# Performance work log

Measured on AMD Instinct MI355X. Metric: run time of the kernel, lower is better.

The kernel has to match this reference:

```python
import jax, jax.numpy as jnp
import numpy as np

SCALE = 8
NUM_CLASSES = 15
IGNORE_THRES = 0.5
# anchors for scale=8 divided by scale
GRID_ANCHOR = jnp.array([[96.0 / 8, 230.0 / 8], [79.0 / 8, 186.0 / 8], [81.0 / 8, 133.0 / 8]], dtype=jnp.float32)  # [3,2]


def _bce_sum(p, t, mask):
    # torch BCELoss(reduction='sum') with log clamped at -100, restricted to mask
    lp = jnp.maximum(jnp.log(p), -100.0)
    ln = jnp.maximum(jnp.log(1.0 - p), -100.0)
    return jnp.sum(-(t * lp + (1.0 - t) * ln) * mask)


def setup_inputs() -> dict:
    key = jax.random.key(0)
    k1, k2, k3 = jax.random.split(key, 3)
    nB, nG = 128, 52
    x = jax.random.normal(k1, (nB, 3 * (NUM_CLASSES + 5), nG, nG), dtype=jnp.float32)
    boxes = jax.random.uniform(k2, (nB, 4), minval=0.1, maxval=0.6)  # cx,cy,w,h in (0,1)
    cls = jax.random.randint(k3, (nB, 1), 0, NUM_CLASSES).astype(jnp.float32)
    labels = jnp.concatenate([boxes, cls], axis=-1)  # [nB,5]
    return {"x": x, "labels": labels}


def reference(x, labels):
    nB, nG = x.shape[0], x.shape[2]
    pred = x.reshape(nB, 3, NUM_CLASSES + 5, nG, nG).transpose(0, 1, 3, 4, 2)  # [B,3,G,G,20]
    px = jax.nn.sigmoid(pred[..., 0])
    py = jax.nn.sigmoid(pred[..., 1])
    pw = pred[..., 2]
    ph = pred[..., 3]
    conf = jax.nn.sigmoid(pred[..., 4])
    cls = jax.nn.softmax(pred[..., 5:], axis=-1)
    pred_boxs = jnp.stack([px, py, pw, ph], axis=-1)  # [B,3,G,G,4]
    out = jnp.concatenate([
        pred_boxs.reshape(nB, -1, 4) * SCALE,
        conf.reshape(nB, -1, 1),
        cls.reshape(nB, -1, NUM_CLASSES),
    ], axis=-1)

    # ---- build_targets (vectorized; one target per image as in original loop) ----
    tb = labels[:, :4] * nG  # boxes in grid units [B,4]
    gx, gy, gw, gh = tb[:, 0], tb[:, 1], tb[:, 2], tb[:, 3]
    gi = gx.astype(jnp.int32)
    gj = gy.astype(jnp.int32)
    gcls = labels[:, 4].astype(jnp.int32)

    # wh-IoU anchors vs targets -> [3,B]
    aw, ah = GRID_ANCHOR[:, 0:1], GRID_ANCHOR[:, 1:2]
    inter_wh = jnp.minimum(aw, gw[None, :]) * jnp.minimum(ah, gh[None, :])
    ious = inter_wh / (aw * ah + 1e-16 + gw[None, :] * gh[None, :] - inter_wh)
    best_idx = jnp.argmax(ious, axis=0)  # [B]

    bidx = jnp.arange(nB)
    shape4 = (nB, 3, nG, nG)
    obj = jnp.zeros(shape4, jnp.float32).at[bidx, best_idx, gj, gi].set(1.0)

    noobj = jnp.ones(shape4, jnp.float32)
    arep = jnp.tile(jnp.arange(3), nB)
    brep = jnp.repeat(bidx, 3)
    jrep = jnp.repeat(gj, 3)
    irep = jnp.repeat(gi, 3)
    ign = (jnp.reshape(ious.T, (-1,)) > IGNORE_THRES).astype(jnp.float32)
    noobj = noobj.at[brep, arep, jrep, irep].mul(1.0 - ign)
    noobj = noobj.at[bidx, best_idx, gj, gi].set(0.0)

    gif = gi.astype(jnp.float32)
    gjf = gj.astype(jnp.float32)
    tx = jnp.zeros(shape4, jnp.float32).at[bidx, best_idx, gj, gi].set(gx - gif)
    ty = jnp.zeros(shape4, jnp.float32).at[bidx, best_idx, gj, gi].set(gy - gjf)
    tw = jnp.zeros(shape4, jnp.float32).at[bidx, best_idx, gj, gi].set(jnp.log(gw / GRID_ANCHOR[best_idx, 0] + 1e-16))
    th = jnp.zeros(shape4, jnp.float32).at[bidx, best_idx, gj, gi].set(jnp.log(gh / GRID_ANCHOR[best_idx, 1] + 1e-16))
    tcls = jnp.zeros(shape4 + (NUM_CLASSES,), jnp.float32).at[bidx, best_idx, gj, gi, gcls].set(1.0)

    # cls_mask: does argmax of predicted class at target cell match gt class
    pred_cls_at = cls[bidx, best_idx, gj, gi]  # [B,15]
    cls_hit = (jnp.argmax(pred_cls_at, axis=-1) == gcls).astype(jnp.float32)
    cls_mask = jnp.zeros(shape4, jnp.float32).at[bidx, best_idx, gj, gi].set(cls_hit)

    # iou between pred box at target cell and target box (cxcywh, +1 corner convention)
    pb = pred_boxs[bidx, best_idx, gj, gi]  # [B,4]
    b1x1, b1y1 = pb[:, 0] - pb[:, 2] / 2, pb[:, 1] - pb[:, 3] / 2
    b1x2, b1y2 = pb[:, 0] + pb[:, 2] / 2, pb[:, 1] + pb[:, 3] / 2
    b2x1, b2y1 = gx - gw / 2, gy - gh / 2
    b2x2, b2y2 = gx + gw / 2, gy + gh / 2
    iw = jnp.clip(jnp.minimum(b1x2, b2x2) - jnp.maximum(b1x1, b2x1) + 1, 0)
    ih = jnp.clip(jnp.minimum(b1y2, b2y2) - jnp.maximum(b1y1, b2y1) + 1, 0)
    inter = iw * ih
    a1 = (b1x2 - b1x1 + 1) * (b1y2 - b1y1 + 1)
    a2 = (b2x2 - b2x1 + 1) * (b2y2 - b2y1 + 1)
    iou_vec = inter / (a1 + a2 - inter + 1e-16)
    iou_scores = jnp.zeros(shape4, jnp.float32).at[bidx, best_idx, gj, gi].set(iou_vec)

    tconf = obj
    # ---- losses (boolean-mask indexing replaced by masked sums) ----
    loss_x = jnp.sum(jnp.abs(px - tx) * obj)
    loss_y = jnp.sum(jnp.abs(py - ty) * obj)
    loss_w = jnp.sum(jnp.abs(pw - tw) * obj)
    loss_h = jnp.sum(jnp.abs(ph - th) * obj)
    loss_conf = _bce_sum(conf, tconf, obj) + 100.0 * _bce_sum(conf, tconf, noobj)
    loss_cls = _bce_sum(cls, tcls, obj[..., None])
    loss = loss_x + loss_y + loss_w + loss_h + loss_conf + loss_cls
    return (loss, out)
```

## Files before the change

kernel.cpp:

```cpp
#include <hip/hip_runtime.h>
#include <math.h>

#define NB    128
#define NG    52
#define NGG   2704
#define NA    3
#define NCLS  15
#define NCH   20
#define NQ    8112
#define TOTAL 1038336
#define BLK   128
#define NBLK  (TOTAL/BLK)
#define FPB   (BLK*NCH)
#define NQUAD ((FPB-4)/4)

typedef float f4 __attribute__((ext_vector_type(4)));

__global__ __launch_bounds__(BLK) void main_kernel(const float* __restrict__ x,
                                                   const float* __restrict__ labels,
                                                   float* __restrict__ out,
                                                   float* __restrict__ partials) {
    __shared__ __align__(16) float sm[FPB];
    __shared__ float wred[BLK/64];

    int t = threadIdx.x;
    int cell = blockIdx.x * BLK + t;
    int b  = cell / NQ;
    int r  = cell - b * NQ;
    int a  = r / NGG;
    int ji = r - a * NGG;

    const float* __restrict__ xp = x + ((size_t)(b*60 + a*20)) * NGG + ji;
    float z[NCH];
    #pragma unroll
    for (int c = 0; c < NCH; c++) z[c] = xp[c * NGG];

    float v[NCH];
    float conf = 1.0f / (1.0f + __expf(-z[4]));
    v[0] = 8.0f / (1.0f + __expf(-z[0]));
    v[1] = 8.0f / (1.0f + __expf(-z[1]));
    v[2] = 8.0f * z[2];
    v[3] = 8.0f * z[3];
    v[4] = conf;
    float m = z[5];
    #pragma unroll
    for (int c = 6; c < NCH; c++) m = fmaxf(m, z[c]);
    float s = 0.0f;
    #pragma unroll
    for (int c = 0; c < NCLS; c++) { v[5+c] = __expf(z[5+c] - m); s += v[5+c]; }
    float inv = 1.0f / s;
    #pragma unroll
    for (int c = 0; c < NCLS; c++) v[5+c] *= inv;

    float gx = labels[b*5+0] * (float)NG;
    float gy = labels[b*5+1] * (float)NG;
    float gw = labels[b*5+2] * (float)NG;
    float gh = labels[b*5+3] * (float)NG;
    int  gcls = (int)labels[b*5+4];
    int gi = (int)gx, gj = (int)gy;
    float gwgh = gw * gh;
    float i0 = fminf(12.0f,   gw) * fminf(28.75f,  gh);
    float i1 = fminf(9.875f,  gw) * fminf(23.25f,  gh);
    float i2 = fminf(10.125f, gw) * fminf(16.625f, gh);
    float iou0 = i0 / (345.0f      + 1e-16f + gwgh - i0);
    float iou1 = i1 / (229.59375f  + 1e-16f + gwgh - i1);
    float iou2 = i2 / (168.328125f + 1e-16f + gwgh - i2);
    int best = 0; float bv = iou0;
    if (iou1 > bv) { best = 1; bv = iou1; }
    if (iou2 > bv) { best = 2; bv = iou2; }
    float ioua = (a == 0) ? iou0 : ((a == 1) ? iou1 : iou2);
    bool at_t   = (ji == gj * NG + gi);
    bool isbest = (a == best);

    float tsum = 0.0f;
    if (!(at_t && (isbest || ioua > 0.5f)))
        tsum = -100.0f * fmaxf(__logf(1.0f - conf), -100.0f);
    if (at_t && isbest) {
        tsum += -fmaxf(__logf(conf), -100.0f);
        float txv = gx - (float)gi;
        float tyv = gy - (float)gj;
        float abw = (best == 0) ? 12.0f  : ((best == 1) ? 9.875f : 10.125f);
        float abh = (best == 0) ? 28.75f : ((best == 1) ? 23.25f : 16.625f);
        float twv = __logf(gw / abw + 1e-16f);
        float thv = __logf(gh / abh + 1e-16f);
        tsum += fabsf(v[0]*0.125f - txv) + fabsf(v[1]*0.125f - tyv)
              + fabsf(v[2]*0.125f - twv) + fabsf(v[3]*0.125f - thv);
        #pragma unroll
        for (int c = 0; c < NCLS; c++) {
            float p = v[5+c];
            tsum += (c == gcls) ? -fmaxf(__logf(p),        -100.0f)
                                : -fmaxf(__logf(1.0f - p), -100.0f);
        }
    }

    int base = t * NCH - 3;
    #pragma unroll
    for (int c = 0; c < NCH; c++) {
        int L = base + c;
        if (L < 0) L += FPB;
        sm[L] = v[c];
    }

    #pragma unroll
    for (int off = 32; off > 0; off >>= 1) tsum += __shfl_down(tsum, off, 64);
    if ((t & 63) == 0) wred[t >> 6] = tsum;

    __syncthreads();

    size_t gbase = (size_t)blockIdx.x * FPB;
    f4* __restrict__ op = (f4*)(out + gbase + 4);
    const f4* __restrict__ sp = (const f4*)sm;
    #pragma unroll
    for (int k = 0; k < 5; k++) {
        int q = k * BLK + t;
        if (q < NQUAD) __builtin_nontemporal_store(sp[q], &op[q]);
    }
    if (t == 0) {
        out[gbase + 1]   = sm[FPB - 3];
        out[gbase + 2]   = sm[FPB - 2];
        out[gbase + 3]   = sm[FPB - 1];
        out[gbase + FPB] = sm[FPB - 4];
        partials[blockIdx.x] = wred[0] + wred[1];
    }
}

__global__ void finish_kernel(const float* __restrict__ partials,
                              float* __restrict__ out) {
    int t = threadIdx.x;
    float s = 0.0f;
    for (int q = t; q < NBLK; q += 256) s += partials[q];
    __shared__ float red[256];
    red[t] = s;
    __syncthreads();
    for (int k = 128; k > 0; k >>= 1) {
        if (t < k) red[t] += red[t + k];
        __syncthreads();
    }
    if (t == 0) out[0] = red[0];
}

extern "C" void kernel_launch(void* const* d_in, const int* in_sizes, int n_in,
                              void* d_out, int out_size, void* d_ws, size_t ws_size,
                              hipStream_t stream) {
    const float* x      = (const float*)d_in[0];
    const float* labels = (const float*)d_in[1];
    float* out = (float*)d_out;
    float* ws  = (float*)d_ws;

    hipLaunchKernelGGL(main_kernel,   dim3(NBLK), dim3(BLK), 0, stream, x, labels, out, ws);
    hipLaunchKernelGGL(finish_kernel, dim3(1),    dim3(256), 0, stream, ws, out);
}
```

Before: 160.6 us.

## Fuse final loss reduction into main kernel with fixed-point atomics

Removes the separate single-block finish kernel. Each block now adds its partial loss into a 64-bit fixed-point accumulator with an atomic, and the last block to arrive, found through an atomic counter, writes the total. This saves a second kernel launch and its serial reduction, at the cost of a memset of the workspace before each launch and a fixed-point rounding of each partial. The block size is also doubled to 256, which halves the number of blocks and atomics.

```diff
diff --git a/kernel.cpp b/kernel.cpp
--- a/kernel.cpp
+++ b/kernel.cpp
@@ -9,17 +9,19 @@
 #define NCH   20
 #define NQ    8112
 #define TOTAL 1038336
-#define BLK   128
+#define BLK   256
 #define NBLK  (TOTAL/BLK)
 #define FPB   (BLK*NCH)
 #define NQUAD ((FPB-4)/4)
 
 typedef float f4 __attribute__((ext_vector_type(4)));
 
+#define FIXSCALE 4294967296.0
+
 __global__ __launch_bounds__(BLK) void main_kernel(const float* __restrict__ x,
                                                    const float* __restrict__ labels,
                                                    float* __restrict__ out,
-                                                   float* __restrict__ partials) {
+                                                   unsigned long long* __restrict__ ws) {
     __shared__ __align__(16) float sm[FPB];
     __shared__ float wred[BLK/64];
 
@@ -115,28 +117,26 @@
         int q = k * BLK + t;
         if (q < NQUAD) __builtin_nontemporal_store(sp[q], &op[q]);
     }
+
     if (t == 0) {
         out[gbase + 1]   = sm[FPB - 3];
         out[gbase + 2]   = sm[FPB - 2];
         out[gbase + 3]   = sm[FPB - 1];
         out[gbase + FPB] = sm[FPB - 4];
-        partials[blockIdx.x] = wred[0] + wred[1];
+
+        float part = wred[0] + wred[1] + wred[2] + wred[3];
+        long long fx = (long long)((double)part * FIXSCALE);
+        atomicAdd(ws, (unsigned long long)fx);
+        __threadfence();
+        unsigned int* cnt = (unsigned int*)(ws + 1);
+        unsigned int old = atomicAdd(cnt, 1u);
+        if (old == NBLK - 1) {
+            __threadfence();
+            unsigned long long acc = atomicAdd(ws, 0ULL);
+            double total = (double)(long long)acc * (1.0 / FIXSCALE);
+            out[0] = (float)total;
+        }
     }
-}
-
-__global__ void finish_kernel(const float* __restrict__ partials,
-                              float* __restrict__ out) {
-    int t = threadIdx.x;
-    float s = 0.0f;
-    for (int q = t; q < NBLK; q += 256) s += partials[q];
-    __shared__ float red[256];
-    red[t] = s;
-    __syncthreads();
-    for (int k = 128; k > 0; k >>= 1) {
-        if (t < k) red[t] += red[t + k];
-        __syncthreads();
-    }
-    if (t == 0) out[0] = red[0];
 }
 
 extern "C" void kernel_launch(void* const* d_in, const int* in_sizes, int n_in,
@@ -145,8 +145,9 @@
     const float* x      = (const float*)d_in[0];
     const float* labels = (const float*)d_in[1];
     float* out = (float*)d_out;
-    float* ws  = (float*)d_ws;
+    unsigned long long* ws = (unsigned long long*)d_ws;
 
-    hipLaunchKernelGGL(main_kernel,   dim3(NBLK), dim3(BLK), 0, stream, x, labels, out, ws);
-    hipLaunchKernelGGL(finish_kernel, dim3(1),    dim3(256), 0, stream, ws, out);
+    hipMemsetAsync(d_ws, 0, 16, stream);
+    hipLaunchKernelGGL(main_kernel, dim3(NBLK), dim3(BLK), 0, stream,
+                       x, labels, out, ws);
 }
```

New measurement: 347.5 us. 116% more time.

## Make output staging per-wavefront and drop block barrier, widen final reduction

Applied to the files above, without the earlier changes.

Each 64-lane wavefront now stages its own 20-channel outputs in a private shared-memory slice and writes them out without a block-wide __syncthreads. The loss partial is stored per wavefront, so the block-level wave reduction goes away. Block size doubles to 256, and the finish kernel uses 1024 threads to sum the larger partials array. This removes block barrier stalls at the cost of more partial sums and smaller coalesced store segments per wave.

```diff
diff --git a/kernel.cpp b/kernel.cpp
--- a/kernel.cpp
+++ b/kernel.cpp
@@ -9,10 +9,11 @@
 #define NCH   20
 #define NQ    8112
 #define TOTAL 1038336
-#define BLK   128
+#define BLK   256
 #define NBLK  (TOTAL/BLK)
-#define FPB   (BLK*NCH)
-#define NQUAD ((FPB-4)/4)
+#define WPB   (BLK/64)
+#define FPW   (64*NCH)
+#define NPART (NBLK*WPB)
 
 typedef float f4 __attribute__((ext_vector_type(4)));
 
@@ -20,10 +21,11 @@
                                                    const float* __restrict__ labels,
                                                    float* __restrict__ out,
                                                    float* __restrict__ partials) {
-    __shared__ __align__(16) float sm[FPB];
-    __shared__ float wred[BLK/64];
+    __shared__ __align__(16) float sm[WPB][FPW];
 
     int t = threadIdx.x;
+    int w = t >> 6;
+    int l = t & 63;
     int cell = blockIdx.x * BLK + t;
     int b  = cell / NQ;
     int r  = cell - b * NQ;
@@ -93,46 +95,49 @@
         }
     }
 
-    int base = t * NCH - 3;
+    float* __restrict__ smw = sm[w];
+    int base = l * NCH - 3;
     #pragma unroll
     for (int c = 0; c < NCH; c++) {
         int L = base + c;
-        if (L < 0) L += FPB;
-        sm[L] = v[c];
+        if (L < 0) L += FPW;
+        smw[L] = v[c];
     }
 
     #pragma unroll
     for (int off = 32; off > 0; off >>= 1) tsum += __shfl_down(tsum, off, 64);
-    if ((t & 63) == 0) wred[t >> 6] = tsum;
 
-    __syncthreads();
-
-    size_t gbase = (size_t)blockIdx.x * FPB;
-    f4* __restrict__ op = (f4*)(out + gbase + 4);
-    const f4* __restrict__ sp = (const f4*)sm;
+    int cell0 = blockIdx.x * BLK + w * 64;
+    size_t gf = 1 + (size_t)cell0 * NCH;
+    f4* __restrict__ op = (f4*)(out + gf + 3);
+    const f4* __restrict__ sp = (const f4*)smw;
     #pragma unroll
     for (int k = 0; k < 5; k++) {
-        int q = k * BLK + t;
-        if (q < NQUAD) __builtin_nontemporal_store(sp[q], &op[q]);
+        int q = k * 64 + l;
+        if (q < (FPW - 4) / 4) __builtin_nontemporal_store(sp[q], &op[q]);
     }
-    if (t == 0) {
-        out[gbase + 1]   = sm[FPB - 3];
-        out[gbase + 2]   = sm[FPB - 2];
-        out[gbase + 3]   = sm[FPB - 1];
-        out[gbase + FPB] = sm[FPB - 4];
-        partials[blockIdx.x] = wred[0] + wred[1];
+    if (l == 0) {
+        out[gf + 0]       = smw[FPW - 3];
+        out[gf + 1]       = smw[FPW - 2];
+        out[gf + 2]       = smw[FPW - 1];
+        out[gf + FPW - 1] = smw[FPW - 4];
+        partials[blockIdx.x * WPB + w] = tsum;
     }
 }
 
-__global__ void finish_kernel(const float* __restrict__ partials,
-                              float* __restrict__ out) {
+__global__ __launch_bounds__(1024) void finish_kernel(const float* __restrict__ partials,
+                                                      float* __restrict__ out) {
     int t = threadIdx.x;
     float s = 0.0f;
-    for (int q = t; q < NBLK; q += 256) s += partials[q];
-    __shared__ float red[256];
+    #pragma unroll
+    for (int k = 0; k < NPART/1024 + 1; k++) {
+        int q = k * 1024 + t;
+        if (q < NPART) s += partials[q];
+    }
+    __shared__ float red[1024];
     red[t] = s;
     __syncthreads();
-    for (int k = 128; k > 0; k >>= 1) {
+    for (int k = 512; k > 0; k >>= 1) {
         if (t < k) red[t] += red[t + k];
         __syncthreads();
     }
@@ -147,6 +152,6 @@
     float* out = (float*)d_out;
     float* ws  = (float*)d_ws;
 
-    hipLaunchKernelGGL(main_kernel,   dim3(NBLK), dim3(BLK), 0, stream, x, labels, out, ws);
-    hipLaunchKernelGGL(finish_kernel, dim3(1),    dim3(256), 0, stream, ws, out);
+    hipLaunchKernelGGL(main_kernel,   dim3(NBLK), dim3(BLK),  0, stream, x, labels, out, ws);
+    hipLaunchKernelGGL(finish_kernel, dim3(1),    dim3(1024), 0, stream, ws, out);
 }
```

New measurement: 154.8 us, median of 2. 3.6% less time.
